# Performance work log

Measured on AMD Instinct MI355X. Metric: run time of the kernel, lower is better.

Reference implementation:

```python
import jax, jax.numpy as jnp
import numpy as np

N = 3600      # nodes (pinned by h0/c0 shape in the torch module)
H = 512       # lstm_hidden
PES = 588     # pes feature width (LSTM input size)
PROT = 384    # protein feature width
OC = 256      # out_channels
E = 230400    # edges (avg degree 64)


def _lstm_cell(x, h, c, wih, whh, bih, bhh):
    # single-timestep PyTorch LSTM cell; gate order i, f, g, o
    g = x @ wih.T + h @ whh.T + bih + bhh
    i, f, gg, o = jnp.split(g, 4, axis=-1)
    c2 = jax.nn.sigmoid(f) * c + jax.nn.sigmoid(i) * jnp.tanh(gg)
    return jax.nn.sigmoid(o) * jnp.tanh(c2)


def _gcn(x, rows, cols, norm, W, b):
    # PyG GCNConv: X' = D^{-1/2}(A+I)D^{-1/2} X W + b
    xw = x @ W
    return jax.ops.segment_sum(xw[rows] * norm[:, None], cols, num_segments=N) + b


def setup_inputs() -> dict:
    key = jax.random.key(0)
    ks = jax.random.split(key, 24)
    s = 0.05
    d = {
        "x": jax.random.normal(ks[0], (N, PES + PROT), jnp.float32),
        "edge_index": jax.random.randint(ks[1], (2, E), 0, N),
        "h0": jax.random.normal(ks[2], (4, N, H), jnp.float32),
        "c0": jax.random.normal(ks[3], (4, N, H), jnp.float32),
    }
    ins = [PES, PES, 2 * H, 2 * H]
    names = ["l0f", "l0b", "l1f", "l1b"]
    for i, (nm, di) in enumerate(zip(names, ins)):
        d["wih" + nm] = jax.random.normal(ks[4 + 4 * i], (4 * H, di), jnp.float32) * s
        d["whh" + nm] = jax.random.normal(ks[5 + 4 * i], (4 * H, H), jnp.float32) * s
        d["bih" + nm] = jnp.zeros((4 * H,), jnp.float32)
        d["bhh" + nm] = jnp.zeros((4 * H,), jnp.float32)
    d["W1"] = jax.random.normal(ks[20], (PROT + 2 * H, 2 * OC), jnp.float32) * s
    d["b1"] = jnp.zeros((2 * OC,), jnp.float32)
    d["W2"] = jax.random.normal(ks[21], (2 * OC, OC), jnp.float32) * s
    d["b2"] = jnp.zeros((OC,), jnp.float32)
    return d


def reference(x, edge_index, h0, c0,
              wihl0f, whhl0f, bihl0f, bhhl0f,
              wihl0b, whhl0b, bihl0b, bhhl0b,
              wihl1f, whhl1f, bihl1f, bhhl1f,
              wihl1b, whhl1b, bihl1b, bhhl1b,
              W1, b1, W2, b2):
    pes = x[:, :PES]
    prot = x[:, PES:]
    # BiLSTM over seq_len=1: one cell step per direction per layer
    hf = _lstm_cell(pes, h0[0], c0[0], wihl0f, whhl0f, bihl0f, bhhl0f)
    hb = _lstm_cell(pes, h0[1], c0[1], wihl0b, whhl0b, bihl0b, bhhl0b)
    x1 = jnp.concatenate([hf, hb], axis=1)
    hf2 = _lstm_cell(x1, h0[2], c0[2], wihl1f, whhl1f, bihl1f, bhhl1f)
    hb2 = _lstm_cell(x1, h0[3], c0[3], wihl1b, whhl1b, bihl1b, bhhl1b)
    x_p = jnp.concatenate([hf2, hb2], axis=1) / 100.0
    feat = jnp.concatenate([prot, x_p], axis=1)  # dropout is identity in eval
    # add self-loops, symmetric normalization
    loop = jnp.arange(N)
    rows = jnp.concatenate([edge_index[0], loop])
    cols = jnp.concatenate([edge_index[1], loop])
    deg = jax.ops.segment_sum(jnp.ones_like(rows, jnp.float32), cols, num_segments=N)
    dinv = jax.lax.rsqrt(deg)  # deg >= 1 because of self-loops
    norm = dinv[rows] * dinv[cols]
    h1 = jax.nn.relu(_gcn(feat, rows, cols, norm, W1, b1))
    return _gcn(h1, rows, cols, norm, W2, b2)
```

## Files before the change

### kernel.cpp

```cpp
#include <hip/hip_runtime.h>
#include <hip/hip_bf16.h>

#define NN 3600
#define MP 3712
#define KADJ 3616
#define NH (3600*512)
#define EE 230400
#define NKT0 9
#define NKT1 12

typedef __hip_bfloat16 bf16;
typedef __bf16 bf16x8 __attribute__((ext_vector_type(8)));
typedef float f32x4 __attribute__((ext_vector_type(4)));
typedef int i32x8 __attribute__((ext_vector_type(8)));
typedef unsigned char u8x16 __attribute__((ext_vector_type(16)));

typedef __attribute__((address_space(1))) void as1v;
typedef __attribute__((address_space(3))) void as3v;

__device__ __forceinline__ void glds16(void* lds, const void* g) {
  __builtin_amdgcn_global_load_lds((as1v*)(void*)g, (as3v*)lds, 16, 0, 0);
}

__device__ __forceinline__ float sigm(float v) { return 1.0f / (1.0f + expf(-v)); }

__device__ __forceinline__ unsigned char f2fp8(float f) {
  return (unsigned char)(__builtin_amdgcn_cvt_pk_fp8_f32(f, 0.f, 0, false) & 0xff);
}

template<int MODE>
__global__ __launch_bounds__(256) void gemm_lstm8(
    const unsigned char* __restrict__ Af, const unsigned char* __restrict__ Bf,
    const float* __restrict__ c0f, const float* __restrict__ bihf,
    const float* __restrict__ bhhf,
    const unsigned char* __restrict__ Ab, const unsigned char* __restrict__ Bb,
    const float* __restrict__ c0b, const float* __restrict__ bihb,
    const float* __restrict__ bhhb,
    void* __restrict__ dst1, void* __restrict__ dst2,
    int nkt, int hx)
{
  __shared__ alignas(16) unsigned char smem[32768];
  const bool back = (int)blockIdx.x >= hx;
  const unsigned char* A = back ? Ab : Af;
  const unsigned char* B = back ? Bb : Bf;
  const float* c0  = back ? c0b : c0f;
  const float* bih = back ? bihb : bihf;
  const float* bhh = back ? bhhb : bhhf;
  const int t = threadIdx.x, w = t >> 6, l = t & 63;
  const int nblk = back ? (int)blockIdx.x - hx : (int)blockIdx.x;
  const unsigned char* gA = A + (((size_t)blockIdx.y * nkt) << 14) + t*16;
  const unsigned char* gB = B + (((size_t)nblk * nkt) << 14) + t*16;
  unsigned char* lA = smem + w*1024;
  unsigned char* lB = smem + 16384 + w*1024;
  const int wm = (w>>1)*64, wn = (w&1)*64;
  const int kb = l >> 4;
  const int aoff = kb*4096 + (wm + (l&15))*32;
  const int boff = 16384 + kb*4096 + (wn + (l&15))*32;
  f32x4 acc[4][4] = {};
  for (int kt = 0; kt < nkt; ++kt) {
    const size_t ko = (size_t)kt << 14;
    __syncthreads();
    glds16(lA,          gA + ko);
    glds16(lA + 4096,   gA + ko + 4096);
    glds16(lA + 8192,   gA + ko + 8192);
    glds16(lA + 12288,  gA + ko + 12288);
    glds16(lB,          gB + ko);
    glds16(lB + 4096,   gB + ko + 4096);
    glds16(lB + 8192,   gB + ko + 8192);
    glds16(lB + 12288,  gB + ko + 12288);
    __syncthreads();
    i32x8 av[4], bv[4];
#pragma unroll
    for (int mi = 0; mi < 4; ++mi) av[mi] = *(const i32x8*)(smem + aoff + mi*512);
#pragma unroll
    for (int ni = 0; ni < 4; ++ni) bv[ni] = *(const i32x8*)(smem + boff + ni*512);
#pragma unroll
    for (int mi = 0; mi < 4; ++mi)
#pragma unroll
      for (int ni = 0; ni < 4; ++ni)
        acc[mi][ni] = __builtin_amdgcn_mfma_scale_f32_16x16x128_f8f6f4(
            av[mi], bv[ni], acc[mi][ni], 0, 0, 0, 127, 0, 127);
  }
  const int jh = (((nblk << 7) + wn) >> 2) + (l & 15);
  const float bI = bih[jh]        + bhh[jh];
  const float bF = bih[512 + jh]  + bhh[512 + jh];
  const float bG = bih[1024 + jh] + bhh[1024 + jh];
  const float bO = bih[1536 + jh] + bhh[1536 + jh];
  const int crow = ((int)blockIdx.y << 7) + wm + ((l>>4)<<2);
  const int kk = (back ? 512 : 0) + jh;
  const size_t kpart = ((size_t)(kk >> 7) << 14) + ((size_t)((kk >> 5) & 3) << 12) + (kk & 31);
  const int colOff = back ? 896 : 384;
#pragma unroll
  for (int mi = 0; mi < 4; ++mi)
#pragma unroll
    for (int jr = 0; jr < 4; ++jr) {
      const int n = crow + mi*16 + jr;
      if (n < NN) {
        const float gi = acc[mi][0][jr] + bI;
        const float gf = acc[mi][1][jr] + bF;
        const float gg = acc[mi][2][jr] + bG;
        const float go = acc[mi][3][jr] + bO;
        const float c2 = sigm(gf) * c0[(size_t)n*512 + jh] + sigm(gi) * tanhf(gg);
        const float h  = sigm(go) * tanhf(c2);
        if (MODE == 0) {
          const unsigned char h8 = f2fp8(h);
          const size_t off = (((size_t)(n >> 7) * NKT1) << 14) + kpart + ((size_t)(n & 127) << 5);
          ((unsigned char*)dst1)[off] = h8;
          ((unsigned char*)dst2)[off] = h8;
        } else {
          ((bf16*)dst1)[(size_t)n*1408 + colOff + jh] = __float2bfloat16(h * 0.01f);
        }
      }
    }
}

__global__ __launch_bounds__(256) void gemm_bt_sk(const bf16* __restrict__ A,
                                                  const bf16* __restrict__ B,
                                                  float* __restrict__ Cp,
                                                  int Kp, int ldc, int ksteps)
{
  __shared__ alignas(16) char smem[16384];
  const int t = threadIdx.x, w = t >> 6, l = t & 63;
  const int mbase = blockIdx.y << 7, nbase = blockIdx.x << 7;
  const int total = Kp >> 5;
  const int kstart = blockIdx.z * ksteps;
  int steps = total - kstart; if (steps > ksteps) steps = ksteps;
  const size_t ldb = (size_t)Kp * 2;
  const char* gA = (const char*)A + (size_t)(mbase + w*16 + (l>>2)) * ldb
                   + (size_t)((l&3)*16) + (size_t)kstart*64;
  const char* gB = (const char*)B + (size_t)(nbase + w*16 + (l>>2)) * ldb
                   + (size_t)((l&3)*16) + (size_t)kstart*64;
  char* lA = smem + w*1024;
  char* lB = smem + 8192 + w*1024;
  const int wm = (w>>1)*64, wn = (w&1)*64;
  const int aoff = (wm + (l&15))*64 + (l>>4)*16;
  const int boff = 8192 + (wn + (l&15))*64 + (l>>4)*16;
  f32x4 acc[4][4] = {};
  const size_t chunk = ldb * 64;
  for (int kt = 0; kt < steps; ++kt) {
    const size_t ko = (size_t)kt * 64;
    __syncthreads();
    glds16(lA,        gA + ko);
    glds16(lA + 4096, gA + ko + chunk);
    glds16(lB,        gB + ko);
    glds16(lB + 4096, gB + ko + chunk);
    __syncthreads();
    bf16x8 av[4], bv[4];
#pragma unroll
    for (int mi = 0; mi < 4; ++mi) av[mi] = *(const bf16x8*)(smem + aoff + mi*1024);
#pragma unroll
    for (int ni = 0; ni < 4; ++ni) bv[ni] = *(const bf16x8*)(smem + boff + ni*1024);
#pragma unroll
    for (int mi = 0; mi < 4; ++mi)
#pragma unroll
      for (int ni = 0; ni < 4; ++ni)
        acc[mi][ni] = __builtin_amdgcn_mfma_f32_16x16x32_bf16(av[mi], bv[ni], acc[mi][ni], 0, 0, 0);
  }
  float* Cz = Cp + (size_t)blockIdx.z * ((size_t)(gridDim.y << 7) * ldc);
  const int crow = mbase + wm + ((l>>4)<<2);
  const int ccol = nbase + wn + (l&15);
#pragma unroll
  for (int mi = 0; mi < 4; ++mi)
#pragma unroll
    for (int ni = 0; ni < 4; ++ni) {
      float* cp = Cz + (size_t)(crow + mi*16)*ldc + (ccol + ni*16);
#pragma unroll
      for (int j = 0; j < 4; ++j) cp[(size_t)j*ldc] = acc[mi][ni][j];
    }
}

__global__ void reduce_bf_pad(const float* __restrict__ p, bf16* __restrict__ dst, int Z)
{
  int k = blockIdx.x*256 + threadIdx.x;
  int r = blockIdx.y;
  if (k >= KADJ) return;
  const size_t psz = (size_t)gridDim.y * MP;
  float s = 0.f;
  if (k < NN)
    for (int z = 0; z < Z; ++z) s += p[(size_t)z*psz + (size_t)r*MP + k];
  dst[(size_t)r*KADJ + k] = __float2bfloat16(s);
}

__global__ void reduce_relu_bf(const float* __restrict__ p, const float* __restrict__ b,
                               bf16* __restrict__ dst)
{
  int idx = blockIdx.x*256 + threadIdx.x;
  int f = idx & 511;
  float s = b[f];
#pragma unroll
  for (int z = 0; z < 4; ++z) s += p[(size_t)z*MP*512 + idx];
  dst[idx] = __float2bfloat16(fmaxf(s, 0.f));
}

__global__ void reduce_bias_out(const float* __restrict__ p, const float* __restrict__ b,
                                float* __restrict__ out)
{
  int idx = blockIdx.x*256 + threadIdx.x;
  if (idx >= NN*256) return;
  int f = idx & 255;
  float s = b[f];
#pragma unroll
  for (int z = 0; z < 8; ++z) s += p[(size_t)z*MP*256 + idx];
  out[idx] = s;
}

__global__ void pack_B_8(const float* __restrict__ wih, const float* __restrict__ whh,
                         unsigned char* __restrict__ dst, int kx, int nkt)
{
  const int kt = blockIdx.x >> 2, kbId = blockIdx.x & 3;
  const int t = threadIdx.x;
  const int r = t >> 1, kio = (t & 1) << 4;
  const int R = ((int)blockIdx.y << 7) + r;
  const int src = (((R >> 4) & 3) << 9) + ((R >> 6) << 4) + (R & 15);
  const int kbase = kt*128 + kbId*32 + kio;
  u8x16 v;
#pragma unroll
  for (int i = 0; i < 16; ++i) {
    const int k = kbase + i;
    float f = 0.f;
    if (k < kx) f = wih[(size_t)src*kx + k];
    else if (k < kx + 512) f = whh[(size_t)src*512 + (k - kx)];
    v[i] = f2fp8(f);
  }
  *(u8x16*)(dst + (((size_t)blockIdx.y*nkt + kt) << 14) + (kbId << 12) + (r << 5) + kio) = v;
}

__global__ void pack_A0_8(const float* __restrict__ x, const float* __restrict__ h0,
                          unsigned char* __restrict__ a0f, unsigned char* __restrict__ a0b)
{
  const int kt = blockIdx.x >> 2, kbId = blockIdx.x & 3;
  const int t = threadIdx.x;
  const int r = t >> 1, kio = (t & 1) << 4;
  const int n = ((int)blockIdx.y << 7) + r;
  const int kbase = kt*128 + kbId*32 + kio;
  const float* hsrc = h0 + (size_t)blockIdx.z * NH;
  u8x16 v;
#pragma unroll
  for (int i = 0; i < 16; ++i) {
    const int k = kbase + i;
    float f = 0.f;
    if (n < NN) {
      if (k < 588) f = x[(size_t)n*972 + k];
      else if (k < 1100) f = hsrc[(size_t)n*512 + (k - 588)];
    }
    v[i] = f2fp8(f);
  }
  unsigned char* dst = blockIdx.z ? a0b : a0f;
  *(u8x16*)(dst + (((size_t)blockIdx.y*NKT0 + kt) << 14) + (kbId << 12) + (r << 5) + kio) = v;
}

__global__ void pack_A1h_8(const float* __restrict__ h0,
                           unsigned char* __restrict__ a1f, unsigned char* __restrict__ a1b)
{
  const int kt = 8 + (blockIdx.x >> 2), kbId = blockIdx.x & 3;
  const int t = threadIdx.x;
  const int r = t >> 1, kio = (t & 1) << 4;
  const int n = ((int)blockIdx.y << 7) + r;
  const int kbase = kt*128 + kbId*32 + kio;
  const float* hsrc = h0 + (size_t)(2 + blockIdx.z) * NH;
  u8x16 v;
#pragma unroll
  for (int i = 0; i < 16; ++i) {
    const int k = kbase + i;
    float f = (n < NN) ? hsrc[(size_t)n*512 + (k - 1024)] : 0.f;
    v[i] = f2fp8(f);
  }
  unsigned char* dst = blockIdx.z ? a1b : a1f;
  *(u8x16*)(dst + (((size_t)blockIdx.y*NKT1 + kt) << 14) + (kbId << 12) + (r << 5) + kio) = v;
}

__global__ void pack_BT(const float* __restrict__ W, bf16* __restrict__ dst, int Nc, int K)
{
  int k = blockIdx.x*256 + threadIdx.x;
  int n = blockIdx.y;
  if (k >= K) return;
  dst[(size_t)n*K + k] = __float2bfloat16(W[(size_t)k*Nc + n]);
}

__global__ void pack_prot(const float* __restrict__ x, bf16* __restrict__ afeat)
{
  int k = blockIdx.x*256 + threadIdx.x;
  int n = blockIdx.y;
  if (k >= 384) return;
  float v = (n < NN) ? x[(size_t)n*972 + 588 + k] : 0.f;
  afeat[(size_t)n*1408 + k] = __float2bfloat16(v);
}

__global__ void deg_count(const int* __restrict__ ecols, int* __restrict__ deg)
{
  int e = blockIdx.x*256 + threadIdx.x;
  if (e < EE) atomicAdd(&deg[ecols[e]], 1);
}

__global__ void calc_dinv(const int* __restrict__ deg, float* __restrict__ dinv)
{
  int n = blockIdx.x*256 + threadIdx.x;
  if (n < NN) dinv[n] = 1.0f / sqrtf((float)(deg[n] + 1));
}

__global__ void adj_scatter(const int* __restrict__ er, const int* __restrict__ ec,
                            const float* __restrict__ dinv, float* __restrict__ adjf)
{
  int e = blockIdx.x*256 + threadIdx.x;
  if (e < EE) {
    int r = er[e], c = ec[e];
    atomicAdd(&adjf[(size_t)c*KADJ + r], dinv[r]*dinv[c]);
  } else if (e < EE + NN) {
    int n = e - EE;
    float d = dinv[n];
    atomicAdd(&adjf[(size_t)n*KADJ + n], d*d);
  }
}

__global__ void cvt_bf(const float* __restrict__ src, int lds,
                       bf16* __restrict__ dst, int rv, int kv)
{
  int k = blockIdx.x*256 + threadIdx.x;
  int r = blockIdx.y;
  if (k >= KADJ) return;
  float v = (r < rv && k < kv) ? src[(size_t)r*lds + k] : 0.f;
  dst[(size_t)r*KADJ + k] = __float2bfloat16(v);
}

#define OFF_DEG   ((size_t)0)
#define OFF_DINV  ((size_t)16384)
#define OFF_BW2   ((size_t)32768)
#define OFF_B0F   ((size_t)294912)
#define OFF_B0B   ((size_t)4882432)
#define OFF_B1F   ((size_t)9469952)
#define OFF_B1B   ((size_t)15761408)
#define OFF_BW1   ((size_t)22052864)
#define OFF_A0F   ((size_t)23494656)
#define OFF_A0B   ((size_t)31809536)
#define OFF_A1F   ((size_t)40124416)
#define OFF_A1B   ((size_t)51527680)
#define OFF_G     ((size_t)62930944)
#define OFF_AFEAT OFF_A0F
#define OFF_XW1P  OFF_G
#define OFF_XWT1B OFF_B0F
#define OFF_ADJF  ((size_t)40124416)
#define OFF_ADJB  ((size_t)4194304)
#define OFF_H1P   ((size_t)40124416)
#define OFF_H1    ((size_t)70533120)
#define OFF_XW2P  ((size_t)74334208)
#define OFF_XWT2B ((size_t)89538560)
#define OFF_O2P   ((size_t)40124416)

extern "C" void kernel_launch(void* const* d_in, const int* in_sizes, int n_in,
                              void* d_out, int out_size, void* d_ws, size_t ws_size,
                              hipStream_t stream)
{
  const float* x    = (const float*)d_in[0];
  const int*   ei   = (const int*)d_in[1];
  const float* h0   = (const float*)d_in[2];
  const float* c0   = (const float*)d_in[3];
  const float* wih0f = (const float*)d_in[4];
  const float* whh0f = (const float*)d_in[5];
  const float* bih0f = (const float*)d_in[6];
  const float* bhh0f = (const float*)d_in[7];
  const float* wih0b = (const float*)d_in[8];
  const float* whh0b = (const float*)d_in[9];
  const float* bih0b = (const float*)d_in[10];
  const float* bhh0b = (const float*)d_in[11];
  const float* wih1f = (const float*)d_in[12];
  const float* whh1f = (const float*)d_in[13];
  const float* bih1f = (const float*)d_in[14];
  const float* bhh1f = (const float*)d_in[15];
  const float* wih1b = (const float*)d_in[16];
  const float* whh1b = (const float*)d_in[17];
  const float* bih1b = (const float*)d_in[18];
  const float* bhh1b = (const float*)d_in[19];
  const float* W1 = (const float*)d_in[20];
  const float* b1 = (const float*)d_in[21];
  const float* W2 = (const float*)d_in[22];
  const float* b2 = (const float*)d_in[23];

  char* ws = (char*)d_ws;
  int*   deg  = (int*)(ws + OFF_DEG);
  float* dinv = (float*)(ws + OFF_DINV);
  unsigned char* B0f8 = (unsigned char*)(ws + OFF_B0F);
  unsigned char* B0b8 = (unsigned char*)(ws + OFF_B0B);
  unsigned char* B1f8 = (unsigned char*)(ws + OFF_B1F);
  unsigned char* B1b8 = (unsigned char*)(ws + OFF_B1B);
  bf16* BW1 = (bf16*)(ws + OFF_BW1);
  bf16* BW2 = (bf16*)(ws + OFF_BW2);
  unsigned char* A0f8 = (unsigned char*)(ws + OFF_A0F);
  unsigned char* A0b8 = (unsigned char*)(ws + OFF_A0B);
  unsigned char* A1f8 = (unsigned char*)(ws + OFF_A1F);
  unsigned char* A1b8 = (unsigned char*)(ws + OFF_A1B);
  bf16* Afeat = (bf16*)(ws + OFF_AFEAT);
  float* xw1p  = (float*)(ws + OFF_XW1P);
  bf16*  xwt1b = (bf16*)(ws + OFF_XWT1B);
  float* adjf  = (float*)(ws + OFF_ADJF);
  bf16*  adjb  = (bf16*)(ws + OFF_ADJB);
  float* h1p   = (float*)(ws + OFF_H1P);
  bf16*  h1bf  = (bf16*)(ws + OFF_H1);
  float* xw2p  = (float*)(ws + OFF_XW2P);
  bf16*  xwt2b = (bf16*)(ws + OFF_XWT2B);
  float* o2p   = (float*)(ws + OFF_O2P);
  float* outp = (float*)d_out;

  hipMemsetAsync(deg, 0, (size_t)NN*4, stream);
  deg_count<<<dim3((EE+255)/256), 256, 0, stream>>>(ei + EE, deg);
  calc_dinv<<<dim3(15), 256, 0, stream>>>(deg, dinv);

  pack_B_8<<<dim3(NKT0*4, 16), 256, 0, stream>>>(wih0f, whh0f, B0f8, 588, NKT0);
  pack_B_8<<<dim3(NKT0*4, 16), 256, 0, stream>>>(wih0b, whh0b, B0b8, 588, NKT0);
  pack_B_8<<<dim3(NKT1*4, 16), 256, 0, stream>>>(wih1f, whh1f, B1f8, 1024, NKT1);
  pack_B_8<<<dim3(NKT1*4, 16), 256, 0, stream>>>(wih1b, whh1b, B1b8, 1024, NKT1);
  pack_BT<<<dim3(6, 512), 256, 0, stream>>>(W1, BW1, 512, 1408);
  pack_BT<<<dim3(2, 256), 256, 0, stream>>>(W2, BW2, 256, 512);

  pack_A0_8<<<dim3(NKT0*4, 29, 2), 256, 0, stream>>>(x, h0, A0f8, A0b8);
  pack_A1h_8<<<dim3(16, 29, 2), 256, 0, stream>>>(h0, A1f8, A1b8);

  gemm_lstm8<0><<<dim3(32, 29), 256, 0, stream>>>(
      A0f8, B0f8, c0,              bih0f, bhh0f,
      A0b8, B0b8, c0 + (size_t)NH, bih0b, bhh0b,
      A1f8, A1b8, NKT0, 16);

  pack_prot<<<dim3(2, MP), 256, 0, stream>>>(x, Afeat);

  gemm_lstm8<1><<<dim3(32, 29), 256, 0, stream>>>(
      A1f8, B1f8, c0 + (size_t)2*NH, bih1f, bhh1f,
      A1b8, B1b8, c0 + (size_t)3*NH, bih1b, bhh1b,
      Afeat, nullptr, NKT1, 16);

  gemm_bt_sk<<<dim3(29, 4, 4), 256, 0, stream>>>(BW1, Afeat, xw1p, 1408, MP, 11);
  reduce_bf_pad<<<dim3(15, 512), 256, 0, stream>>>(xw1p, xwt1b, 4);

  hipMemsetAsync(adjf, 0, (size_t)NN*KADJ*4, stream);
  adj_scatter<<<dim3((EE+NN+255)/256), 256, 0, stream>>>(ei, ei + EE, dinv, adjf);
  cvt_bf<<<dim3(15, MP), 256, 0, stream>>>(adjf, KADJ, adjb, NN, KADJ);

  gemm_bt_sk<<<dim3(4, 29, 4), 256, 0, stream>>>(adjb, xwt1b, h1p, KADJ, 512, 29);
  reduce_relu_bf<<<dim3(MP*512/256), 256, 0, stream>>>(h1p, b1, h1bf);

  gemm_bt_sk<<<dim3(29, 2, 4), 256, 0, stream>>>(BW2, h1bf, xw2p, 512, MP, 4);
  reduce_bf_pad<<<dim3(15, 256), 256, 0, stream>>>(xw2p, xwt2b, 4);

  gemm_bt_sk<<<dim3(2, 29, 8), 256, 0, stream>>>(adjb, xwt2b, o2p, KADJ, 256, 15);
  reduce_bias_out<<<dim3(3600), 256, 0, stream>>>(o2p, b2, outp);
}
```

Measured before the change: 354.8 us.

## Double-buffer LDS tiles in fp8 LSTM GEMM and bf16 split-K GEMM

Both GEMM kernels now keep two LDS buffers and issue the global-to-LDS loads for the next K tile before running the MFMAs on the current one. This replaces the two barriers per iteration with one and is meant to hide global load latency behind compute. LDS use doubles (64KB for the fp8 kernel), which can lower occupancy. The barrier placement relies on the async global_load_lds having completed before the single end-of-iteration barrier, and whether the compiler inserts the needed vmcnt wait there is unclear.

Result: faster. 341.4 us (-3.8%).

```diff
diff --git a/kernel.cpp b/kernel.cpp
--- a/kernel.cpp
+++ b/kernel.cpp
@@ -39,7 +39,7 @@
     void* __restrict__ dst1, void* __restrict__ dst2,
     int nkt, int hx)
 {
-  __shared__ alignas(16) unsigned char smem[32768];
+  __shared__ alignas(16) unsigned char smem[65536];
   const bool back = (int)blockIdx.x >= hx;
   const unsigned char* A = back ? Ab : Af;
   const unsigned char* B = back ? Bb : Bf;
@@ -50,16 +50,16 @@
   const int nblk = back ? (int)blockIdx.x - hx : (int)blockIdx.x;
   const unsigned char* gA = A + (((size_t)blockIdx.y * nkt) << 14) + t*16;
   const unsigned char* gB = B + (((size_t)nblk * nkt) << 14) + t*16;
-  unsigned char* lA = smem + w*1024;
-  unsigned char* lB = smem + 16384 + w*1024;
   const int wm = (w>>1)*64, wn = (w&1)*64;
   const int kb = l >> 4;
   const int aoff = kb*4096 + (wm + (l&15))*32;
   const int boff = 16384 + kb*4096 + (wn + (l&15))*32;
   f32x4 acc[4][4] = {};
-  for (int kt = 0; kt < nkt; ++kt) {
+
+  auto STAGE = [&](int buf, int kt) {
+    unsigned char* lA = smem + buf*32768 + w*1024;
+    unsigned char* lB = smem + buf*32768 + 16384 + w*1024;
     const size_t ko = (size_t)kt << 14;
-    __syncthreads();
     glds16(lA,          gA + ko);
     glds16(lA + 4096,   gA + ko + 4096);
     glds16(lA + 8192,   gA + ko + 8192);
@@ -68,18 +68,27 @@
     glds16(lB + 4096,   gB + ko + 4096);
     glds16(lB + 8192,   gB + ko + 8192);
     glds16(lB + 12288,  gB + ko + 12288);
-    __syncthreads();
+  };
+
+  STAGE(0, 0);
+  __syncthreads();
+  int cur = 0;
+  for (int kt = 0; kt < nkt; ++kt) {
+    if (kt + 1 < nkt) STAGE(cur ^ 1, kt + 1);
+    const unsigned char* base = smem + cur*32768;
     i32x8 av[4], bv[4];
 #pragma unroll
-    for (int mi = 0; mi < 4; ++mi) av[mi] = *(const i32x8*)(smem + aoff + mi*512);
-#pragma unroll
-    for (int ni = 0; ni < 4; ++ni) bv[ni] = *(const i32x8*)(smem + boff + ni*512);
+    for (int mi = 0; mi < 4; ++mi) av[mi] = *(const i32x8*)(base + aoff + mi*512);
+#pragma unroll
+    for (int ni = 0; ni < 4; ++ni) bv[ni] = *(const i32x8*)(base + boff + ni*512);
 #pragma unroll
     for (int mi = 0; mi < 4; ++mi)
 #pragma unroll
       for (int ni = 0; ni < 4; ++ni)
         acc[mi][ni] = __builtin_amdgcn_mfma_scale_f32_16x16x128_f8f6f4(
             av[mi], bv[ni], acc[mi][ni], 0, 0, 0, 127, 0, 127);
+    __syncthreads();
+    cur ^= 1;
   }
   const int jh = (((nblk << 7) + wn) >> 2) + (l & 15);
   const float bI = bih[jh]        + bhh[jh];
@@ -119,7 +128,7 @@
                                                   float* __restrict__ Cp,
                                                   int Kp, int ldc, int ksteps)
 {
-  __shared__ alignas(16) char smem[16384];
+  __shared__ alignas(16) char smem[32768];
   const int t = threadIdx.x, w = t >> 6, l = t & 63;
   const int mbase = blockIdx.y << 7, nbase = blockIdx.x << 7;
   const int total = Kp >> 5;
@@ -130,31 +139,40 @@
                    + (size_t)((l&3)*16) + (size_t)kstart*64;
   const char* gB = (const char*)B + (size_t)(nbase + w*16 + (l>>2)) * ldb
                    + (size_t)((l&3)*16) + (size_t)kstart*64;
-  char* lA = smem + w*1024;
-  char* lB = smem + 8192 + w*1024;
   const int wm = (w>>1)*64, wn = (w&1)*64;
   const int aoff = (wm + (l&15))*64 + (l>>4)*16;
   const int boff = 8192 + (wn + (l&15))*64 + (l>>4)*16;
   f32x4 acc[4][4] = {};
   const size_t chunk = ldb * 64;
-  for (int kt = 0; kt < steps; ++kt) {
+
+  auto STAGE = [&](int buf, int kt) {
+    char* lA = smem + buf*16384 + w*1024;
+    char* lB = smem + buf*16384 + 8192 + w*1024;
     const size_t ko = (size_t)kt * 64;
-    __syncthreads();
     glds16(lA,        gA + ko);
     glds16(lA + 4096, gA + ko + chunk);
     glds16(lB,        gB + ko);
     glds16(lB + 4096, gB + ko + chunk);
-    __syncthreads();
+  };
+
+  STAGE(0, 0);
+  __syncthreads();
+  int cur = 0;
+  for (int kt = 0; kt < steps; ++kt) {
+    if (kt + 1 < steps) STAGE(cur ^ 1, kt + 1);
+    const char* base = smem + cur*16384;
     bf16x8 av[4], bv[4];
 #pragma unroll
-    for (int mi = 0; mi < 4; ++mi) av[mi] = *(const bf16x8*)(smem + aoff + mi*1024);
-#pragma unroll
-    for (int ni = 0; ni < 4; ++ni) bv[ni] = *(const bf16x8*)(smem + boff + ni*1024);
+    for (int mi = 0; mi < 4; ++mi) av[mi] = *(const bf16x8*)(base + aoff + mi*1024);
+#pragma unroll
+    for (int ni = 0; ni < 4; ++ni) bv[ni] = *(const bf16x8*)(base + boff + ni*1024);
 #pragma unroll
     for (int mi = 0; mi < 4; ++mi)
 #pragma unroll
       for (int ni = 0; ni < 4; ++ni)
         acc[mi][ni] = __builtin_amdgcn_mfma_f32_16x16x32_bf16(av[mi], bv[ni], acc[mi][ni], 0, 0, 0);
+    __syncthreads();
+    cur ^= 1;
   }
   float* Cz = Cp + (size_t)blockIdx.z * ((size_t)(gridDim.y << 7) * ldc);
   const int crow = mbase + wm + ((l>>4)<<2);
```
